# Kernel tuning notes

Measured on AMD Instinct MI355X. Metric: run time of the kernel, lower is better.

## Reference

```python
import jax, jax.numpy as jnp
import numpy as np

N = 50000      # nodes
E = 800000     # edges (before self loops)
D_IN = 128
D_H = 128
HEADS = 4
C = D_H // HEADS
D_OUT = 64
G = 50         # graphs in batch
EPS = 1e-5


def setup_inputs() -> dict:
    key = jax.random.key(0)
    ks = jax.random.split(key, 40)
    def rn(k, shape, scale=0.05):
        return jax.random.normal(k, shape, jnp.float32) * scale
    inp = {}
    inp['x'] = jax.random.normal(ks[0], (N, D_IN), jnp.float32)
    inp['edge_index'] = jax.random.randint(ks[1], (2, E), 0, N, dtype=jnp.int32)
    inp['batch'] = jnp.sort(jax.random.randint(ks[2], (N,), 0, G, dtype=jnp.int32))
    # GATConv 1 (in=D_IN, heads=4, out-per-head=C, concat)
    inp['gat1_W'] = rn(ks[3], (D_IN, D_H))
    inp['gat1_as'] = rn(ks[4], (HEADS, C))
    inp['gat1_ad'] = rn(ks[5], (HEADS, C))
    inp['gat1_b'] = rn(ks[6], (D_H,))
    # GATConv 2 (in=D_H)
    inp['gat2_W'] = rn(ks[7], (D_H, D_H))
    inp['gat2_as'] = rn(ks[8], (HEADS, C))
    inp['gat2_ad'] = rn(ks[9], (HEADS, C))
    inp['gat2_b'] = rn(ks[10], (D_H,))
    # SAGEConv 3/4/5: lin_l (aggregated neighbors, has bias), lin_r (root, no bias)
    for i, kk in zip((3, 4, 5), (11, 14, 17)):
        inp[f'sage{i}_Wl'] = rn(ks[kk], (D_H, D_H))
        inp[f'sage{i}_bl'] = rn(ks[kk + 1], (D_H,))
        inp[f'sage{i}_Wr'] = rn(ks[kk + 2], (D_H, D_H))
    # BatchNorms (training-mode batch statistics)
    for i in range(1, 6):
        inp[f'bn{i}_g'] = jnp.ones((D_H,), jnp.float32)
        inp[f'bn{i}_b'] = jnp.zeros((D_H,), jnp.float32)
    # residual projections + final fc
    inp['res1_W'] = rn(ks[20], (D_IN, D_H)); inp['res1_b'] = rn(ks[21], (D_H,))
    inp['res2_W'] = rn(ks[22], (D_H, D_H)); inp['res2_b'] = rn(ks[23], (D_H,))
    inp['fc_W'] = rn(ks[24], (D_H, D_OUT)); inp['fc_b'] = rn(ks[25], (D_OUT,))
    return inp


def _segsum(v, idx, n):
    return jax.ops.segment_sum(v, idx, num_segments=n)


def _gat(x, W, a_src, a_dst, b, src, dst):
    # PyG GATConv with self loops already appended to (src, dst).
    h = (x @ W).reshape(N, HEADS, C)
    es = jnp.einsum('nhc,hc->nh', h, a_src)           # [N,H]
    ed = jnp.einsum('nhc,hc->nh', h, a_dst)
    e = jax.nn.leaky_relu(es[src] + ed[dst], 0.2)     # [Etot,H]
    m = jax.ops.segment_max(e, dst, num_segments=N)
    m = jnp.where(jnp.isfinite(m), m, 0.0)
    w = jnp.exp(e - m[dst])
    z = _segsum(w, dst, N)
    alpha = w / jnp.maximum(z[dst], 1e-16)            # edge softmax over dst
    out = _segsum(h[src] * alpha[:, :, None], dst, N)  # [N,H,C]
    return out.reshape(N, D_H) + b


def _sage(x, Wl, bl, Wr, src, dst):
    # PyG SAGEConv(aggr='mean'): lin_l(mean_neighbors) + lin_r(x)
    deg = _segsum(jnp.ones((src.shape[0],), x.dtype), dst, N)
    mean = _segsum(x[src], dst, N) / jnp.maximum(deg, 1.0)[:, None]
    return mean @ Wl + bl + x @ Wr


def _bn(x, g, b):
    mu = x.mean(0)
    var = x.var(0)
    return g * (x - mu) * jax.lax.rsqrt(var + EPS) + b


def reference(x, edge_index, batch,
              gat1_W, gat1_as, gat1_ad, gat1_b,
              gat2_W, gat2_as, gat2_ad, gat2_b,
              sage3_Wl, sage3_bl, sage3_Wr,
              sage4_Wl, sage4_bl, sage4_Wr,
              sage5_Wl, sage5_bl, sage5_Wr,
              bn1_g, bn1_b, bn2_g, bn2_b, bn3_g, bn3_b, bn4_g, bn4_b, bn5_g, bn5_b,
              res1_W, res1_b, res2_W, res2_b, fc_W, fc_b):
    src, dst = edge_index[0], edge_index[1]
    loops = jnp.arange(N, dtype=edge_index.dtype)
    gsrc = jnp.concatenate([src, loops])   # GATConv adds self loops by default
    gdst = jnp.concatenate([dst, loops])
    lrelu = lambda v: jax.nn.leaky_relu(v, 0.2)

    res1 = x @ res1_W + res1_b
    h = _gat(x, gat1_W, gat1_as, gat1_ad, gat1_b, gsrc, gdst)
    h = lrelu(_bn(h, bn1_g, bn1_b) + res1)            # dropout = identity (eval)

    res2 = h @ res2_W + res2_b
    h = _gat(h, gat2_W, gat2_as, gat2_ad, gat2_b, gsrc, gdst)
    h = lrelu(_bn(h, bn2_g, bn2_b) + res2)

    h = lrelu(_bn(_sage(h, sage3_Wl, sage3_bl, sage3_Wr, src, dst), bn3_g, bn3_b))
    h = lrelu(_bn(_sage(h, sage4_Wl, sage4_bl, sage4_Wr, src, dst), bn4_g, bn4_b))
    h = lrelu(_bn(_sage(h, sage5_Wl, sage5_bl, sage5_Wr, src, dst), bn5_g, bn5_b))

    # global_mean_pool over graphs
    cnt = jax.ops.segment_sum(jnp.ones((N,), h.dtype), batch, num_segments=G)
    pooled = jax.ops.segment_sum(h, batch, num_segments=G) / jnp.maximum(cnt, 1.0)[:, None]
    return pooled @ fc_W + fc_b
```

## Files before the change

### kernel.cpp

```cpp
#include <hip/hip_runtime.h>
#include <math.h>
#include <stdint.h>

#define N_NODES 50000
#define N_EDGES 800000
#define D 128
#define GR 50
#define EPSV 1e-5f

typedef __attribute__((ext_vector_type(8))) short bf16x8;
typedef __attribute__((ext_vector_type(4))) float f32x4;

__device__ __forceinline__ float lrelu(float v){ return v > 0.f ? v : 0.2f*v; }

__device__ __forceinline__ unsigned int f2bf(float f){
  union { float f; uint32_t i; } v; v.f = f;
  uint32_t r = v.i + 0x7fffu + ((v.i >> 16) & 1u);
  return r >> 16;
}
__device__ __forceinline__ float2 bf2f2(uint32_t u){
  union { uint32_t i; float f; } a, b;
  a.i = u << 16;
  b.i = u & 0xffff0000u;
  return make_float2(a.f, b.f);
}

__global__ void k_countrank(const int* __restrict__ dst, int* __restrict__ deg,
                            int* __restrict__ rank){
  int e = blockIdx.x*256 + threadIdx.x;
  if (e < N_EDGES) rank[e] = atomicAdd(&deg[dst[e]], 1);
}
__global__ void k_scan1(const int* __restrict__ deg, int* __restrict__ bsum){
  __shared__ int s[256];
  int i = blockIdx.x*256 + threadIdx.x;
  int v = (i < N_NODES) ? deg[i] : 0;
  s[threadIdx.x] = v; __syncthreads();
  for (int off = 128; off > 0; off >>= 1){
    if (threadIdx.x < off) s[threadIdx.x] += s[threadIdx.x + off];
    __syncthreads();
  }
  if (threadIdx.x == 0) bsum[blockIdx.x] = s[0];
}
__global__ void k_scan2b(int* __restrict__ bsum, int nb, int* __restrict__ rowStart){
  __shared__ int s[256];
  int t = threadIdx.x;
  int v = (t < nb) ? bsum[t] : 0;
  s[t] = v; __syncthreads();
  for (int off = 1; off < 256; off <<= 1){
    int xv = (t >= off) ? s[t - off] : 0;
    __syncthreads();
    s[t] += xv;
    __syncthreads();
  }
  if (t < nb) bsum[t] = s[t] - v;
  if (t == 255) rowStart[N_NODES] = s[255];
}
__global__ void k_scan3(const int* __restrict__ deg, const int* __restrict__ bsum,
                        int* __restrict__ rowStart){
  __shared__ int s[256];
  int i = blockIdx.x*256 + threadIdx.x;
  int v = (i < N_NODES) ? deg[i] : 0;
  s[threadIdx.x] = v; __syncthreads();
  for (int off = 1; off < 256; off <<= 1){
    int xv = (threadIdx.x >= off) ? s[threadIdx.x - off] : 0;
    __syncthreads();
    s[threadIdx.x] += xv;
    __syncthreads();
  }
  if (i < N_NODES) rowStart[i] = bsum[blockIdx.x] + s[threadIdx.x] - v;
}
__global__ void k_scatter(const int* __restrict__ src, const int* __restrict__ dst,
                          const int* __restrict__ rank, const int* __restrict__ rowStart,
                          int* __restrict__ srcList){
  int e = blockIdx.x*256 + threadIdx.x;
  if (e < N_EDGES)
    srcList[rowStart[dst[e]] + rank[e]] = src[e];
}

__global__ void k_cast_x(const float* __restrict__ x, unsigned short* __restrict__ x16){
  int idx = blockIdx.x*256 + threadIdx.x;
  if (idx >= N_NODES*32) return;
  float4 v = *(const float4*)(x + (size_t)idx*4);
  uint2 pk;
  pk.x = f2bf(v.x) | (f2bf(v.y) << 16);
  pk.y = f2bf(v.z) | (f2bf(v.w) << 16);
  *(uint2*)(x16 + (size_t)idx*4) = pk;
}

struct WPack { const float* w[10]; };
__global__ void k_castw(WPack p, unsigned short* __restrict__ wt){
  int mat = blockIdx.x >> 6;
  int local = (blockIdx.x & 63)*256 + threadIdx.x;
  int c = local >> 7, k = local & 127;
  wt[(size_t)mat*16384 + c*128 + k] = (unsigned short)f2bf(p.w[mat][k*128 + c]);
}

__device__ __forceinline__ void stage_w(const unsigned short* __restrict__ wt,
                                        unsigned short* __restrict__ lds, int t){
  #pragma unroll
  for (int i = 0; i < 8; ++i){
    int ch = i*256 + t;
    int col = ch >> 4, kc = ch & 15;
    *(uint4*)(&lds[col*136 + kc*8]) = *(const uint4*)(wt + ((size_t)col << 7) + (kc << 3));
  }
}

__device__ __forceinline__ void mfma_k128(const unsigned short* __restrict__ xrow,
                                          const unsigned short* __restrict__ lds,
                                          int lane, f32x4 acc[8]){
  int quad = lane >> 4, m = lane & 15;
  #pragma unroll
  for (int ks = 0; ks < 4; ++ks){
    bf16x8 a = *(const bf16x8*)(xrow + ks*32 + quad*8);
    #pragma unroll
    for (int nt = 0; nt < 8; ++nt){
      bf16x8 b = *(const bf16x8*)(&lds[(nt*16 + m)*136 + ks*32 + quad*8]);
      acc[nt] = __builtin_amdgcn_mfma_f32_16x16x32_bf16(a, b, acc[nt], 0, 0, 0);
    }
  }
}

__global__ __launch_bounds__(256) void k_mgemm(const unsigned short* __restrict__ X16,
    const unsigned short* __restrict__ wt, const float* __restrict__ bias,
    float* __restrict__ Y, int n){
  __shared__ __align__(16) unsigned short Wlds[128*136];
  int t = threadIdx.x, lane = t & 63, w = t >> 6;
  int quad = lane >> 4, m = lane & 15;
  int rbase = blockIdx.x*64 + w*16;
  stage_w(wt, Wlds, t);
  f32x4 acc[8];
  #pragma unroll
  for (int nt = 0; nt < 8; ++nt){ acc[nt][0]=0.f; acc[nt][1]=0.f; acc[nt][2]=0.f; acc[nt][3]=0.f; }
  int rowA = rbase + m; if (rowA >= n) rowA = n - 1;
  __syncthreads();
  mfma_k128(X16 + (size_t)rowA*128, Wlds, lane, acc);
  #pragma unroll
  for (int nt = 0; nt < 8; ++nt){
    int col = nt*16 + m;
    float bv = bias[col];
    #pragma unroll
    for (int reg = 0; reg < 4; ++reg){
      int row = rbase + quad*4 + reg;
      if (row < n) Y[(size_t)row*128 + col] = acc[nt][reg] + bv;
    }
  }
}

__global__ __launch_bounds__(256) void k_mgemm_gat(const unsigned short* __restrict__ X16,
    const unsigned short* __restrict__ wt, const float* __restrict__ as_,
    const float* __restrict__ ad_, unsigned short* __restrict__ H16,
    float* __restrict__ es, float* __restrict__ ed, int n){
  __shared__ __align__(16) unsigned short Wlds[128*136];
  int t = threadIdx.x, lane = t & 63, w = t >> 6;
  int quad = lane >> 4, m = lane & 15;
  int rbase = blockIdx.x*64 + w*16;
  stage_w(wt, Wlds, t);
  f32x4 acc[8];
  #pragma unroll
  for (int nt = 0; nt < 8; ++nt){ acc[nt][0]=0.f; acc[nt][1]=0.f; acc[nt][2]=0.f; acc[nt][3]=0.f; }
  int rowA = rbase + m; if (rowA >= n) rowA = n - 1;
  __syncthreads();
  mfma_k128(X16 + (size_t)rowA*128, Wlds, lane, acc);

  float asv[8], adv[8];
  #pragma unroll
  for (int nt = 0; nt < 8; ++nt){ asv[nt] = as_[nt*16 + m]; adv[nt] = ad_[nt*16 + m]; }

  #pragma unroll
  for (int reg = 0; reg < 4; ++reg){
    int row = rbase + quad*4 + reg;
    float pe[4], pd[4];
    #pragma unroll
    for (int h = 0; h < 4; ++h){
      pe[h] = acc[2*h][reg]*asv[2*h] + acc[2*h+1][reg]*asv[2*h+1];
      pd[h] = acc[2*h][reg]*adv[2*h] + acc[2*h+1][reg]*adv[2*h+1];
    }
    #pragma unroll
    for (int h = 0; h < 4; ++h){
      pe[h] += __shfl_xor(pe[h], 1); pe[h] += __shfl_xor(pe[h], 2);
      pe[h] += __shfl_xor(pe[h], 4); pe[h] += __shfl_xor(pe[h], 8);
      pd[h] += __shfl_xor(pd[h], 1); pd[h] += __shfl_xor(pd[h], 2);
      pd[h] += __shfl_xor(pd[h], 4); pd[h] += __shfl_xor(pd[h], 8);
    }
    if (m == 0 && row < n){
      #pragma unroll
      for (int h = 0; h < 4; ++h){ es[row*4 + h] = pe[h]; ed[row*4 + h] = pd[h]; }
    }
  }
  #pragma unroll
  for (int nt = 0; nt < 8; ++nt){
    int col = nt*16 + m;
    #pragma unroll
    for (int reg = 0; reg < 4; ++reg){
      int row = rbase + quad*4 + reg;
      if (row < n) H16[(size_t)row*128 + col] = (unsigned short)f2bf(acc[nt][reg]);
    }
  }
}

__global__ __launch_bounds__(256) void k_mgemm2(const unsigned short* __restrict__ Xa,
    const unsigned short* __restrict__ wta, const unsigned short* __restrict__ Xb,
    const unsigned short* __restrict__ wtb, const float* __restrict__ bias,
    float* __restrict__ Y, int n, float* __restrict__ bnsum){
  __shared__ __align__(16) unsigned short Wlds[128*136];
  __shared__ float redS[128], redQ[128];
  int t = threadIdx.x, lane = t & 63, w = t >> 6;
  int quad = lane >> 4, m = lane & 15;
  int rbase = blockIdx.x*64 + w*16;
  if (t < 128){ redS[t] = 0.f; redQ[t] = 0.f; }
  f32x4 acc[8];
  #pragma unroll
  for (int nt = 0; nt < 8; ++nt){ acc[nt][0]=0.f; acc[nt][1]=0.f; acc[nt][2]=0.f; acc[nt][3]=0.f; }
  int rowA = rbase + m; if (rowA >= n) rowA = n - 1;

  stage_w(wta, Wlds, t);
  __syncthreads();
  mfma_k128(Xa + (size_t)rowA*128, Wlds, lane, acc);
  __syncthreads();
  stage_w(wtb, Wlds, t);
  __syncthreads();
  mfma_k128(Xb + (size_t)rowA*128, Wlds, lane, acc);

  #pragma unroll
  for (int nt = 0; nt < 8; ++nt){
    int col = nt*16 + m;
    float bv = bias[col];
    float s = 0.f, q = 0.f;
    #pragma unroll
    for (int reg = 0; reg < 4; ++reg){
      int row = rbase + quad*4 + reg;
      if (row < n){
        float o = acc[nt][reg] + bv;
        Y[(size_t)row*128 + col] = o;
        s += o; q += o*o;
      }
    }
    atomicAdd(&redS[col], s);
    atomicAdd(&redQ[col], q);
  }
  __syncthreads();
  if (t < 128){
    atomicAdd(&bnsum[t],       redS[t]);
    atomicAdd(&bnsum[128 + t], redQ[t]);
  }
}

__global__ __launch_bounds__(256) void k_gat(const unsigned int* __restrict__ h16,
    const float* __restrict__ es, const float* __restrict__ edv,
    const int* __restrict__ rowStart, const int* __restrict__ srcList,
    const float* __restrict__ bias, float* __restrict__ out){
  int i = blockIdx.x*4 + (threadIdx.x >> 6);
  if (i >= N_NODES) return;
  int lane = threadIdx.x & 63;
  int hd = lane >> 4;
  int c  = lane * 2;
  float edi = edv[i*4 + hd];
  float2 self = bf2f2(h16[(size_t)i*64 + lane]);
  float w = __expf(lrelu(es[i*4 + hd] + edi));
  float z = w, acc0 = self.x*w, acc1 = self.y*w;
  int k0 = rowStart[i], ke = rowStart[i + 1];
  int k = k0;
  for (; k + 7 < ke; k += 8){
    int s[8]; uint32_t u[8]; float ev[8];
    #pragma unroll
    for (int j = 0; j < 8; ++j) s[j] = srcList[k + j];
    #pragma unroll
    for (int j = 0; j < 8; ++j) u[j] = h16[(size_t)s[j]*64 + lane];
    #pragma unroll
    for (int j = 0; j < 8; ++j) ev[j] = es[s[j]*4 + hd];
    #pragma unroll
    for (int j = 0; j < 8; ++j){
      float wj = __expf(lrelu(ev[j] + edi));
      float2 v = bf2f2(u[j]);
      z += wj; acc0 += v.x*wj; acc1 += v.y*wj;
    }
  }
  for (; k < ke; ++k){
    int s0 = srcList[k];
    uint32_t u0 = h16[(size_t)s0*64 + lane];
    float w0 = __expf(lrelu(es[s0*4 + hd] + edi));
    float2 v0 = bf2f2(u0);
    z += w0; acc0 += v0.x*w0; acc1 += v0.y*w0;
  }
  float inv = 1.f / z;
  float2 bv = *(const float2*)(bias + c);
  *(float2*)(out + (size_t)i*D + c) = make_float2(acc0*inv + bv.x, acc1*inv + bv.y);
}

__global__ __launch_bounds__(256) void k_sage_mean(const unsigned int* __restrict__ h16,
    const int* __restrict__ rowStart, const int* __restrict__ srcList,
    unsigned int* __restrict__ out16){
  int i = blockIdx.x*4 + (threadIdx.x >> 6);
  if (i >= N_NODES) return;
  int lane = threadIdx.x & 63;
  int k0 = rowStart[i], k1 = rowStart[i + 1];
  float a0 = 0.f, a1 = 0.f;
  int k = k0;
  for (; k + 7 < k1; k += 8){
    int s[8]; uint32_t u[8];
    #pragma unroll
    for (int j = 0; j < 8; ++j) s[j] = srcList[k + j];
    #pragma unroll
    for (int j = 0; j < 8; ++j) u[j] = h16[(size_t)s[j]*64 + lane];
    #pragma unroll
    for (int j = 0; j < 8; ++j){
      float2 v = bf2f2(u[j]);
      a0 += v.x; a1 += v.y;
    }
  }
  for (; k < k1; ++k){
    uint32_t u0 = h16[(size_t)srcList[k]*64 + lane];
    float2 v0 = bf2f2(u0);
    a0 += v0.x; a1 += v0.y;
  }
  int dg = k1 - k0;
  float inv = 1.f / (float)(dg > 0 ? dg : 1);
  out16[(size_t)i*64 + lane] = f2bf(a0*inv) | (f2bf(a1*inv) << 16);
}

__global__ __launch_bounds__(256) void k_bnstat(const float* __restrict__ x,
                                                float* __restrict__ sums){
  int col = threadIdx.x & 127;
  int ro  = threadIdx.x >> 7;
  float s = 0.f, s2 = 0.f;
  for (int r = blockIdx.x*2 + ro; r < N_NODES; r += gridDim.x*2){
    float v = x[(size_t)r*D + col];
    s += v; s2 += v*v;
  }
  __shared__ float rs[256], rq[256];
  rs[threadIdx.x] = s; rq[threadIdx.x] = s2;
  __syncthreads();
  if (threadIdx.x < 128){
    atomicAdd(&sums[col],       rs[threadIdx.x] + rs[threadIdx.x + 128]);
    atomicAdd(&sums[128 + col], rq[threadIdx.x] + rq[threadIdx.x + 128]);
  }
}

__global__ void k_bnapply(const float* __restrict__ x, const float* __restrict__ sums,
    const float* __restrict__ g, const float* __restrict__ b,
    const float* __restrict__ res, float* __restrict__ y,
    unsigned int* __restrict__ y16){
  int f = blockIdx.x*256 + threadIdx.x;
  if (f >= N_NODES*32) return;
  int c = (f & 31) * 4;
  float4 v = *(const float4*)(x + (size_t)f*4);
  float vv[4] = {v.x, v.y, v.z, v.w};
  float rr[4] = {0.f, 0.f, 0.f, 0.f};
  if (res){
    float4 rv = *(const float4*)(res + (size_t)f*4);
    rr[0]=rv.x; rr[1]=rv.y; rr[2]=rv.z; rr[3]=rv.w;
  }
  float o[4];
  const float invn = 1.f / (float)N_NODES;
  #pragma unroll
  for (int j = 0; j < 4; ++j){
    int cc = c + j;
    float mu  = sums[cc] * invn;
    float var = sums[128 + cc] * invn - mu*mu;
    float rs  = rsqrtf(var + EPSV);
    o[j] = lrelu((vv[j] - mu)*rs*g[cc] + b[cc] + rr[j]);
  }
  if (y) *(float4*)(y + (size_t)f*4) = make_float4(o[0], o[1], o[2], o[3]);
  if (y16){
    uint2 pk;
    pk.x = f2bf(o[0]) | (f2bf(o[1]) << 16);
    pk.y = f2bf(o[2]) | (f2bf(o[3]) << 16);
    *(uint2*)(y16 + (size_t)f*2) = pk;
  }
}

__global__ __launch_bounds__(256) void k_pool(const float* __restrict__ h,
    const int* __restrict__ batch, float* __restrict__ pooled,
    float* __restrict__ cnt){
  int col = threadIdx.x & 127;
  int ro  = threadIdx.x >> 7;
  int base = blockIdx.x * 128;
  int g_cur = -1; float acc = 0.f, cacc = 0.f;
  for (int ii = 0; ii < 64; ++ii){
    int r = base + ro + ii*2;
    if (r >= N_NODES) break;
    int g = batch[r];
    if (g != g_cur){
      if (g_cur >= 0){
        atomicAdd(&pooled[g_cur*D + col], acc);
        if (col == 0) atomicAdd(&cnt[g_cur], cacc);
      }
      acc = 0.f; cacc = 0.f; g_cur = g;
    }
    acc  += h[(size_t)r*D + col];
    cacc += 1.f;
  }
  if (g_cur >= 0){
    atomicAdd(&pooled[g_cur*D + col], acc);
    if (col == 0) atomicAdd(&cnt[g_cur], cacc);
  }
}

__global__ void k_fc(const float* __restrict__ pooled, const float* __restrict__ cnt,
    const float* __restrict__ W, const float* __restrict__ b, float* __restrict__ out){
  int idx = blockIdx.x*256 + threadIdx.x;
  if (idx >= GR*64) return;
  int g = idx >> 6, o = idx & 63;
  const float* p = pooled + g*D;
  float s = 0.f;
  for (int c2 = 0; c2 < D; ++c2) s += p[c2] * W[c2*64 + o];
  float inv = 1.f / fmaxf(cnt[g], 1.f);
  out[idx] = s*inv + b[o];
}

extern "C" void kernel_launch(void* const* d_in, const int* in_sizes, int n_in,
                              void* d_out, int out_size, void* d_ws, size_t ws_size,
                              hipStream_t stream){
  (void)in_sizes; (void)n_in; (void)out_size; (void)ws_size;
  const float* x       = (const float*)d_in[0];
  const int*   ei      = (const int*)  d_in[1];
  const int*   batch   = (const int*)  d_in[2];
  const float* gat1_W  = (const float*)d_in[3];
  const float* gat1_as = (const float*)d_in[4];
  const float* gat1_ad = (const float*)d_in[5];
  const float* gat1_b  = (const float*)d_in[6];
  const float* gat2_W  = (const float*)d_in[7];
  const float* gat2_as = (const float*)d_in[8];
  const float* gat2_ad = (const float*)d_in[9];
  const float* gat2_b  = (const float*)d_in[10];
  const float* s3_Wl   = (const float*)d_in[11];
  const float* s3_bl   = (const float*)d_in[12];
  const float* s3_Wr   = (const float*)d_in[13];
  const float* s4_Wl   = (const float*)d_in[14];
  const float* s4_bl   = (const float*)d_in[15];
  const float* s4_Wr   = (const float*)d_in[16];
  const float* s5_Wl   = (const float*)d_in[17];
  const float* s5_bl   = (const float*)d_in[18];
  const float* s5_Wr   = (const float*)d_in[19];
  const float* bn1_g = (const float*)d_in[20]; const float* bn1_b = (const float*)d_in[21];
  const float* bn2_g = (const float*)d_in[22]; const float* bn2_b = (const float*)d_in[23];
  const float* bn3_g = (const float*)d_in[24]; const float* bn3_b = (const float*)d_in[25];
  const float* bn4_g = (const float*)d_in[26]; const float* bn4_b = (const float*)d_in[27];
  const float* bn5_g = (const float*)d_in[28]; const float* bn5_b = (const float*)d_in[29];
  const float* res1_W = (const float*)d_in[30]; const float* res1_b = (const float*)d_in[31];
  const float* res2_W = (const float*)d_in[32]; const float* res2_b = (const float*)d_in[33];
  const float* fc_W   = (const float*)d_in[34]; const float* fc_b   = (const float*)d_in[35];
  float* out = (float*)d_out;

  char* ws = (char*)d_ws;
  size_t off = 0;
  auto alloc = [&](size_t bytes) -> void* {
    void* p = ws + off; off += (bytes + 255) & ~(size_t)255; return p;
  };
  int*   rowStart = (int*)  alloc((N_NODES + 1) * 4);
  int*   deg      = (int*)  alloc((size_t)N_NODES * 4);
  int*   rank     = (int*)  alloc((size_t)N_EDGES * 4);
  int*   srcList  = (int*)  alloc((size_t)N_EDGES * 4);
  int*   bsum     = (int*)  alloc(256 * 4);
  float* bnsums   = (float*)alloc(5 * 256 * 4);
  float* pooled   = (float*)alloc(GR * D * 4);
  float* cnt      = (float*)alloc(64 * 4);
  float* es       = (float*)alloc((size_t)N_NODES * 4 * 4);
  float* edv      = (float*)alloc((size_t)N_NODES * 4 * 4);
  unsigned short* Wt16 = (unsigned short*)alloc(10 * 16384 * 2);
  unsigned short* HX   = (unsigned short*)alloc((size_t)N_NODES * D * 2);
  unsigned short* H16a = (unsigned short*)alloc((size_t)N_NODES * D * 2);
  float* B1 = (float*)alloc((size_t)N_NODES * D * 4);
  float* B3 = (float*)alloc((size_t)N_NODES * D * 4);

  const int* srcE = ei;
  const int* dstE = ei + N_EDGES;
  const int nb = (N_NODES + 255) / 256;
  const int egrid = (N_EDGES + 255) / 256;
  const int mgrid = (N_NODES + 63) / 64;
  const int agrid = (N_NODES + 3) / 4;
  const int bgrid = (N_NODES*32 + 255) / 256;
  const int pgrid = (N_NODES + 127) / 128;

  hipMemsetAsync(deg, 0, (size_t)N_NODES*4, stream);
  hipMemsetAsync(bnsums, 0, (5*256 + GR*D + 64)*4, stream);
  k_countrank<<<egrid, 256, 0, stream>>>(dstE, deg, rank);
  k_scan1<<<nb, 256, 0, stream>>>(deg, bsum);
  k_scan2b<<<1, 256, 0, stream>>>(bsum, nb, rowStart);
  k_scan3<<<nb, 256, 0, stream>>>(deg, bsum, rowStart);
  k_scatter<<<egrid, 256, 0, stream>>>(srcE, dstE, rank, rowStart, srcList);

  WPack wp;
  wp.w[0]=res1_W; wp.w[1]=gat1_W; wp.w[2]=res2_W; wp.w[3]=gat2_W;
  wp.w[4]=s3_Wl;  wp.w[5]=s3_Wr;  wp.w[6]=s4_Wl;  wp.w[7]=s4_Wr;
  wp.w[8]=s5_Wl;  wp.w[9]=s5_Wr;
  k_castw<<<640, 256, 0, stream>>>(wp, Wt16);
  k_cast_x<<<bgrid, 256, 0, stream>>>(x, HX);

  k_mgemm<<<mgrid, 256, 0, stream>>>(HX, Wt16 + 0*16384, res1_b, B1, N_NODES);
  k_mgemm_gat<<<mgrid, 256, 0, stream>>>(HX, Wt16 + 1*16384, gat1_as, gat1_ad,
                                         H16a, es, edv, N_NODES);
  k_gat<<<agrid, 256, 0, stream>>>((const unsigned int*)H16a, es, edv, rowStart, srcList, gat1_b, B3);
  k_bnstat<<<256, 256, 0, stream>>>(B3, bnsums);
  k_bnapply<<<bgrid, 256, 0, stream>>>(B3, bnsums, bn1_g, bn1_b, B1,
                                       nullptr, (unsigned int*)H16a);

  k_mgemm<<<mgrid, 256, 0, stream>>>(H16a, Wt16 + 2*16384, res2_b, B1, N_NODES);
  k_mgemm_gat<<<mgrid, 256, 0, stream>>>(H16a, Wt16 + 3*16384, gat2_as, gat2_ad,
                                         HX, es, edv, N_NODES);
  k_gat<<<agrid, 256, 0, stream>>>((const unsigned int*)HX, es, edv, rowStart, srcList, gat2_b, B3);
  k_bnstat<<<256, 256, 0, stream>>>(B3, bnsums + 256);
  k_bnapply<<<bgrid, 256, 0, stream>>>(B3, bnsums + 256, bn2_g, bn2_b, B1,
                                       nullptr, (unsigned int*)H16a);

  k_sage_mean<<<agrid, 256, 0, stream>>>((const unsigned int*)H16a, rowStart, srcList,
                                         (unsigned int*)HX);
  k_mgemm2<<<mgrid, 256, 0, stream>>>(HX, Wt16 + 4*16384, H16a, Wt16 + 5*16384,
                                      s3_bl, B1, N_NODES, bnsums + 512);
  k_bnapply<<<bgrid, 256, 0, stream>>>(B1, bnsums + 512, bn3_g, bn3_b, nullptr,
                                       nullptr, (unsigned int*)H16a);

  k_sage_mean<<<agrid, 256, 0, stream>>>((const unsigned int*)H16a, rowStart, srcList,
                                         (unsigned int*)HX);
  k_mgemm2<<<mgrid, 256, 0, stream>>>(HX, Wt16 + 6*16384, H16a, Wt16 + 7*16384,
                                      s4_bl, B1, N_NODES, bnsums + 768);
  k_bnapply<<<bgrid, 256, 0, stream>>>(B1, bnsums + 768, bn4_g, bn4_b, nullptr,
                                       nullptr, (unsigned int*)H16a);

  k_sage_mean<<<agrid, 256, 0, stream>>>((const unsigned int*)H16a, rowStart, srcList,
                                         (unsigned int*)HX);
  k_mgemm2<<<mgrid, 256, 0, stream>>>(HX, Wt16 + 8*16384, H16a, Wt16 + 9*16384,
                                      s5_bl, B1, N_NODES, bnsums + 1024);
  k_bnapply<<<bgrid, 256, 0, stream>>>(B1, bnsums + 1024, bn5_g, bn5_b, nullptr,
                                       B3, nullptr);

  k_pool<<<pgrid, 256, 0, stream>>>(B3, batch, pooled, cnt);
  k_fc<<<(GR*64 + 255)/256, 256, 0, stream>>>(pooled, cnt, fc_W, fc_b, out);
}
```

Before: 728.0 us.

## Store intermediate activations in bf16 and coalesce GEMM epilogues through LDS

```diff
diff --git a/kernel.cpp b/kernel.cpp
--- a/kernel.cpp
+++ b/kernel.cpp
@@ -95,6 +95,7 @@
   wt[(size_t)mat*16384 + c*128 + k] = (unsigned short)f2bf(p.w[mat][k*128 + c]);
 }
 
+
 __device__ __forceinline__ void stage_w(const unsigned short* __restrict__ wt,
                                         unsigned short* __restrict__ lds, int t){
   #pragma unroll
@@ -105,45 +106,67 @@
   }
 }
 
-__device__ __forceinline__ void mfma_k128(const unsigned short* __restrict__ xrow,
+__device__ __forceinline__ void load_a(const unsigned short* __restrict__ xrow,
+                                       int quad, bf16x8 a[4]){
+  #pragma unroll
+  for (int ks = 0; ks < 4; ++ks)
+    a[ks] = *(const bf16x8*)(xrow + ks*32 + quad*8);
+}
+
+__device__ __forceinline__ void mfma_regs(const bf16x8 a[4],
                                           const unsigned short* __restrict__ lds,
                                           int lane, f32x4 acc[8]){
   int quad = lane >> 4, m = lane & 15;
   #pragma unroll
   for (int ks = 0; ks < 4; ++ks){
-    bf16x8 a = *(const bf16x8*)(xrow + ks*32 + quad*8);
     #pragma unroll
     for (int nt = 0; nt < 8; ++nt){
       bf16x8 b = *(const bf16x8*)(&lds[(nt*16 + m)*136 + ks*32 + quad*8]);
-      acc[nt] = __builtin_amdgcn_mfma_f32_16x16x32_bf16(a, b, acc[nt], 0, 0, 0);
-    }
+      acc[nt] = __builtin_amdgcn_mfma_f32_16x16x32_bf16(a[ks], b, acc[nt], 0, 0, 0);
+    }
+  }
+}
+
+__device__ __forceinline__ void epi_store16(f32x4 acc[8], const float* bias,
+    unsigned short* __restrict__ ldsw, unsigned short* __restrict__ Y16,
+    int rbase, int lane, int n){
+  int quad = lane >> 4, m = lane & 15;
+  #pragma unroll
+  for (int nt = 0; nt < 8; ++nt){
+    int col = nt*16 + m;
+    float bv = bias ? bias[col] : 0.f;
+    #pragma unroll
+    for (int reg = 0; reg < 4; ++reg)
+      ldsw[(quad*4 + reg)*132 + col] = (unsigned short)f2bf(acc[nt][reg] + bv);
+  }
+  int r = lane >> 2, seg = lane & 3;
+  int grow = rbase + r;
+  if (grow < n){
+    unsigned short* gp = Y16 + (size_t)grow*128 + seg*32;
+    #pragma unroll
+    for (int j = 0; j < 4; ++j)
+      *(uint4*)(gp + j*8) = *(const uint4*)(&ldsw[r*132 + seg*32 + j*8]);
   }
 }
 
 __global__ __launch_bounds__(256) void k_mgemm(const unsigned short* __restrict__ X16,
     const unsigned short* __restrict__ wt, const float* __restrict__ bias,
-    float* __restrict__ Y, int n){
+    unsigned short* __restrict__ Y16, int n){
   __shared__ __align__(16) unsigned short Wlds[128*136];
   int t = threadIdx.x, lane = t & 63, w = t >> 6;
   int quad = lane >> 4, m = lane & 15;
   int rbase = blockIdx.x*64 + w*16;
+  int rowA = rbase + m; if (rowA >= n) rowA = n - 1;
+  bf16x8 a[4];
+  load_a(X16 + (size_t)rowA*128, quad, a);
   stage_w(wt, Wlds, t);
   f32x4 acc[8];
   #pragma unroll
   for (int nt = 0; nt < 8; ++nt){ acc[nt][0]=0.f; acc[nt][1]=0.f; acc[nt][2]=0.f; acc[nt][3]=0.f; }
-  int rowA = rbase + m; if (rowA >= n) rowA = n - 1;
-  __syncthreads();
-  mfma_k128(X16 + (size_t)rowA*128, Wlds, lane, acc);
-  #pragma unroll
-  for (int nt = 0; nt < 8; ++nt){
-    int col = nt*16 + m;
-    float bv = bias[col];
-    #pragma unroll
-    for (int reg = 0; reg < 4; ++reg){
-      int row = rbase + quad*4 + reg;
-      if (row < n) Y[(size_t)row*128 + col] = acc[nt][reg] + bv;
-    }
-  }
+  __syncthreads();
+  mfma_regs(a, Wlds, lane, acc);
+  __syncthreads();
+  epi_store16(acc, bias, Wlds + w*2112, Y16, rbase, lane, n);
 }
 
 __global__ __launch_bounds__(256) void k_mgemm_gat(const unsigned short* __restrict__ X16,
@@ -154,18 +177,19 @@
   int t = threadIdx.x, lane = t & 63, w = t >> 6;
   int quad = lane >> 4, m = lane & 15;
   int rbase = blockIdx.x*64 + w*16;
+  int rowA = rbase + m; if (rowA >= n) rowA = n - 1;
+  bf16x8 a[4];
+  load_a(X16 + (size_t)rowA*128, quad, a);
   stage_w(wt, Wlds, t);
   f32x4 acc[8];
   #pragma unroll
   for (int nt = 0; nt < 8; ++nt){ acc[nt][0]=0.f; acc[nt][1]=0.f; acc[nt][2]=0.f; acc[nt][3]=0.f; }
-  int rowA = rbase + m; if (rowA >= n) rowA = n - 1;
-  __syncthreads();
-  mfma_k128(X16 + (size_t)rowA*128, Wlds, lane, acc);
+  __syncthreads();
+  mfma_regs(a, Wlds, lane, acc);
 
   float asv[8], adv[8];
   #pragma unroll
   for (int nt = 0; nt < 8; ++nt){ asv[nt] = as_[nt*16 + m]; adv[nt] = ad_[nt*16 + m]; }
-
   #pragma unroll
   for (int reg = 0; reg < 4; ++reg){
     int row = rbase + quad*4 + reg;
@@ -187,68 +211,80 @@
       for (int h = 0; h < 4; ++h){ es[row*4 + h] = pe[h]; ed[row*4 + h] = pd[h]; }
     }
   }
-  #pragma unroll
-  for (int nt = 0; nt < 8; ++nt){
-    int col = nt*16 + m;
-    #pragma unroll
-    for (int reg = 0; reg < 4; ++reg){
-      int row = rbase + quad*4 + reg;
-      if (row < n) H16[(size_t)row*128 + col] = (unsigned short)f2bf(acc[nt][reg]);
-    }
-  }
+  __syncthreads();
+  epi_store16(acc, nullptr, Wlds + w*2112, H16, rbase, lane, n);
 }
 
 __global__ __launch_bounds__(256) void k_mgemm2(const unsigned short* __restrict__ Xa,
     const unsigned short* __restrict__ wta, const unsigned short* __restrict__ Xb,
     const unsigned short* __restrict__ wtb, const float* __restrict__ bias,
-    float* __restrict__ Y, int n, float* __restrict__ bnsum){
+    unsigned short* __restrict__ Y16, int n, float* __restrict__ bnpart){
   __shared__ __align__(16) unsigned short Wlds[128*136];
-  __shared__ float redS[128], redQ[128];
+  __shared__ float wredS[4][128], wredQ[4][128];
   int t = threadIdx.x, lane = t & 63, w = t >> 6;
   int quad = lane >> 4, m = lane & 15;
   int rbase = blockIdx.x*64 + w*16;
-  if (t < 128){ redS[t] = 0.f; redQ[t] = 0.f; }
+  int rowA = rbase + m; if (rowA >= n) rowA = n - 1;
+  bf16x8 aa[4], ab[4];
+  load_a(Xa + (size_t)rowA*128, quad, aa);
+  load_a(Xb + (size_t)rowA*128, quad, ab);
+  stage_w(wta, Wlds, t);
   f32x4 acc[8];
   #pragma unroll
   for (int nt = 0; nt < 8; ++nt){ acc[nt][0]=0.f; acc[nt][1]=0.f; acc[nt][2]=0.f; acc[nt][3]=0.f; }
-  int rowA = rbase + m; if (rowA >= n) rowA = n - 1;
-
-  stage_w(wta, Wlds, t);
-  __syncthreads();
-  mfma_k128(Xa + (size_t)rowA*128, Wlds, lane, acc);
+  __syncthreads();
+  mfma_regs(aa, Wlds, lane, acc);
   __syncthreads();
   stage_w(wtb, Wlds, t);
   __syncthreads();
-  mfma_k128(Xb + (size_t)rowA*128, Wlds, lane, acc);
-
+  mfma_regs(ab, Wlds, lane, acc);
+
+  float colS[8], colQ[8];
   #pragma unroll
   for (int nt = 0; nt < 8; ++nt){
-    int col = nt*16 + m;
-    float bv = bias[col];
+    float bv = bias[nt*16 + m];
     float s = 0.f, q = 0.f;
     #pragma unroll
     for (int reg = 0; reg < 4; ++reg){
-      int row = rbase + quad*4 + reg;
-      if (row < n){
-        float o = acc[nt][reg] + bv;
-        Y[(size_t)row*128 + col] = o;
-        s += o; q += o*o;
-      }
-    }
-    atomicAdd(&redS[col], s);
-    atomicAdd(&redQ[col], q);
+      float o = acc[nt][reg] + bv;
+      acc[nt][reg] = o;
+      if (rbase + quad*4 + reg < n){ s += o; q += o*o; }
+    }
+    s += __shfl_xor(s, 16); s += __shfl_xor(s, 32);
+    q += __shfl_xor(q, 16); q += __shfl_xor(q, 32);
+    colS[nt] = s; colQ[nt] = q;
+  }
+  if (quad == 0){
+    #pragma unroll
+    for (int nt = 0; nt < 8; ++nt){
+      wredS[w][nt*16 + m] = colS[nt];
+      wredQ[w][nt*16 + m] = colQ[nt];
+    }
   }
   __syncthreads();
   if (t < 128){
-    atomicAdd(&bnsum[t],       redS[t]);
-    atomicAdd(&bnsum[128 + t], redQ[t]);
-  }
+    float S = wredS[0][t] + wredS[1][t] + wredS[2][t] + wredS[3][t];
+    float Q = wredQ[0][t] + wredQ[1][t] + wredQ[2][t] + wredQ[3][t];
+    bnpart[(size_t)blockIdx.x*256 + t]       = S;
+    bnpart[(size_t)blockIdx.x*256 + 128 + t] = Q;
+  }
+  epi_store16(acc, nullptr, Wlds + w*2112, Y16, rbase, lane, n);
+}
+
+__global__ void k_bnred(const float* __restrict__ part, int nblk,
+                        float* __restrict__ sums){
+  int g = blockIdx.x, t = threadIdx.x;
+  int chunk = (nblk + 63) / 64;
+  int b0 = g*chunk, b1 = min(nblk, b0 + chunk);
+  float s = 0.f;
+  for (int b = b0; b < b1; ++b) s += part[(size_t)b*256 + t];
+  if (b0 < b1) atomicAdd(&sums[t], s);
 }
 
 __global__ __launch_bounds__(256) void k_gat(const unsigned int* __restrict__ h16,
     const float* __restrict__ es, const float* __restrict__ edv,
     const int* __restrict__ rowStart, const int* __restrict__ srcList,
-    const float* __restrict__ bias, float* __restrict__ out){
+    const float* __restrict__ bias, unsigned int* __restrict__ out16){
   int i = blockIdx.x*4 + (threadIdx.x >> 6);
   if (i >= N_NODES) return;
   int lane = threadIdx.x & 63;
@@ -284,7 +320,7 @@
   }
   float inv = 1.f / z;
   float2 bv = *(const float2*)(bias + c);
-  *(float2*)(out + (size_t)i*D + c) = make_float2(acc0*inv + bv.x, acc1*inv + bv.y);
+  out16[(size_t)i*64 + lane] = f2bf(acc0*inv + bv.x) | (f2bf(acc1*inv + bv.y) << 16);
 }
 
 __global__ __launch_bounds__(256) void k_sage_mean(const unsigned int* __restrict__ h16,
@@ -309,8 +345,7 @@
     }
   }
   for (; k < k1; ++k){
-    uint32_t u0 = h16[(size_t)srcList[k]*64 + lane];
-    float2 v0 = bf2f2(u0);
+    float2 v0 = bf2f2(h16[(size_t)srcList[k]*64 + lane]);
     a0 += v0.x; a1 += v0.y;
   }
   int dg = k1 - k0;
@@ -318,37 +353,46 @@
   out16[(size_t)i*64 + lane] = f2bf(a0*inv) | (f2bf(a1*inv) << 16);
 }
 
-__global__ __launch_bounds__(256) void k_bnstat(const float* __restrict__ x,
+__global__ __launch_bounds__(256) void k_bnstat(const unsigned int* __restrict__ x16,
                                                 float* __restrict__ sums){
-  int col = threadIdx.x & 127;
-  int ro  = threadIdx.x >> 7;
-  float s = 0.f, s2 = 0.f;
-  for (int r = blockIdx.x*2 + ro; r < N_NODES; r += gridDim.x*2){
-    float v = x[(size_t)r*D + col];
-    s += v; s2 += v*v;
-  }
-  __shared__ float rs[256], rq[256];
-  rs[threadIdx.x] = s; rq[threadIdx.x] = s2;
-  __syncthreads();
-  if (threadIdx.x < 128){
-    atomicAdd(&sums[col],       rs[threadIdx.x] + rs[threadIdx.x + 128]);
-    atomicAdd(&sums[128 + col], rq[threadIdx.x] + rq[threadIdx.x + 128]);
-  }
-}
-
-__global__ void k_bnapply(const float* __restrict__ x, const float* __restrict__ sums,
-    const float* __restrict__ g, const float* __restrict__ b,
-    const float* __restrict__ res, float* __restrict__ y,
+  int colu = threadIdx.x & 63;
+  int ro   = threadIdx.x >> 6;
+  float s0 = 0.f, s1 = 0.f, q0 = 0.f, q1 = 0.f;
+  for (int r = blockIdx.x*4 + ro; r < N_NODES; r += gridDim.x*4){
+    float2 v = bf2f2(x16[(size_t)r*64 + colu]);
+    s0 += v.x; s1 += v.y; q0 += v.x*v.x; q1 += v.y*v.y;
+  }
+  __shared__ float rs0[256], rs1[256], rq0[256], rq1[256];
+  int t = threadIdx.x;
+  rs0[t] = s0; rs1[t] = s1; rq0[t] = q0; rq1[t] = q1;
+  __syncthreads();
+  if (t < 64){
+    float S0 = rs0[t] + rs0[t+64] + rs0[t+128] + rs0[t+192];
+    float S1 = rs1[t] + rs1[t+64] + rs1[t+128] + rs1[t+192];
+    float Q0 = rq0[t] + rq0[t+64] + rq0[t+128] + rq0[t+192];
+    float Q1 = rq1[t] + rq1[t+64] + rq1[t+128] + rq1[t+192];
+    atomicAdd(&sums[2*t],       S0);
+    atomicAdd(&sums[2*t + 1],   S1);
+    atomicAdd(&sums[128 + 2*t],     Q0);
+    atomicAdd(&sums[128 + 2*t + 1], Q1);
+  }
+}
+
+__global__ void k_bnapply(const unsigned int* __restrict__ x16,
+    const float* __restrict__ sums, const float* __restrict__ g,
+    const float* __restrict__ b, const unsigned int* __restrict__ res16,
     unsigned int* __restrict__ y16){
   int f = blockIdx.x*256 + threadIdx.x;
   if (f >= N_NODES*32) return;
   int c = (f & 31) * 4;
-  float4 v = *(const float4*)(x + (size_t)f*4);
-  float vv[4] = {v.x, v.y, v.z, v.w};
+  uint2 u = *(const uint2*)(x16 + (size_t)f*2);
+  float2 vA = bf2f2(u.x), vB = bf2f2(u.y);
+  float vv[4] = {vA.x, vA.y, vB.x, vB.y};
   float rr[4] = {0.f, 0.f, 0.f, 0.f};
-  if (res){
-    float4 rv = *(const float4*)(res + (size_t)f*4);
-    rr[0]=rv.x; rr[1]=rv.y; rr[2]=rv.z; rr[3]=rv.w;
+  if (res16){
+    uint2 ur = *(const uint2*)(res16 + (size_t)f*2);
+    float2 rA = bf2f2(ur.x), rB = bf2f2(ur.y);
+    rr[0]=rA.x; rr[1]=rA.y; rr[2]=rB.x; rr[3]=rB.y;
   }
   float o[4];
   const float invn = 1.f / (float)N_NODES;
@@ -360,39 +404,38 @@
     float rs  = rsqrtf(var + EPSV);
     o[j] = lrelu((vv[j] - mu)*rs*g[cc] + b[cc] + rr[j]);
   }
-  if (y) *(float4*)(y + (size_t)f*4) = make_float4(o[0], o[1], o[2], o[3]);
-  if (y16){
-    uint2 pk;
-    pk.x = f2bf(o[0]) | (f2bf(o[1]) << 16);
-    pk.y = f2bf(o[2]) | (f2bf(o[3]) << 16);
-    *(uint2*)(y16 + (size_t)f*2) = pk;
-  }
-}
-
-__global__ __launch_bounds__(256) void k_pool(const float* __restrict__ h,
+  uint2 pk;
+  pk.x = f2bf(o[0]) | (f2bf(o[1]) << 16);
+  pk.y = f2bf(o[2]) | (f2bf(o[3]) << 16);
+  *(uint2*)(y16 + (size_t)f*2) = pk;
+}
+
+__global__ __launch_bounds__(256) void k_pool(const unsigned int* __restrict__ h16,
     const int* __restrict__ batch, float* __restrict__ pooled,
     float* __restrict__ cnt){
-  int col = threadIdx.x & 127;
-  int ro  = threadIdx.x >> 7;
+  int colu = threadIdx.x & 63;
+  int ro   = threadIdx.x >> 6;
   int base = blockIdx.x * 128;
-  int g_cur = -1; float acc = 0.f, cacc = 0.f;
-  for (int ii = 0; ii < 64; ++ii){
-    int r = base + ro + ii*2;
+  int g_cur = -1; float a0 = 0.f, a1 = 0.f, cacc = 0.f;
+  for (int ii = 0; ii < 32; ++ii){
+    int r = base + ro + ii*4;
     if (r >= N_NODES) break;
     int g = batch[r];
     if (g != g_cur){
       if (g_cur >= 0){
-        atomicAdd(&pooled[g_cur*D + col], acc);
-        if (col == 0) atomicAdd(&cnt[g_cur], cacc);
+        atomicAdd(&pooled[g_cur*D + 2*colu],     a0);
+        atomicAdd(&pooled[g_cur*D + 2*colu + 1], a1);
+        if (colu == 0) atomicAdd(&cnt[g_cur], cacc);
       }
-      acc = 0.f; cacc = 0.f; g_cur = g;
-    }
-    acc  += h[(size_t)r*D + col];
-    cacc += 1.f;
+      a0 = 0.f; a1 = 0.f; cacc = 0.f; g_cur = g;
+    }
+    float2 v = bf2f2(h16[(size_t)r*64 + colu]);
+    a0 += v.x; a1 += v.y; cacc += 1.f;
   }
   if (g_cur >= 0){
-    atomicAdd(&pooled[g_cur*D + col], acc);
-    if (col == 0) atomicAdd(&cnt[g_cur], cacc);
+    atomicAdd(&pooled[g_cur*D + 2*colu],     a0);
+    atomicAdd(&pooled[g_cur*D + 2*colu + 1], a1);
+    if (colu == 0) atomicAdd(&cnt[g_cur], cacc);
   }
 }
 
@@ -447,6 +490,7 @@
   auto alloc = [&](size_t bytes) -> void* {
     void* p = ws + off; off += (bytes + 255) & ~(size_t)255; return p;
   };
+  const int mgrid = (N_NODES + 63) / 64;
   int*   rowStart = (int*)  alloc((N_NODES + 1) * 4);
   int*   deg      = (int*)  alloc((size_t)N_NODES * 4);
   int*   rank     = (int*)  alloc((size_t)N_EDGES * 4);
@@ -457,17 +501,17 @@
   float* cnt      = (float*)alloc(64 * 4);
   float* es       = (float*)alloc((size_t)N_NODES * 4 * 4);
   float* edv      = (float*)alloc((size_t)N_NODES * 4 * 4);
+  float* bnpart   = (float*)alloc((size_t)mgrid * 256 * 4);
   unsigned short* Wt16 = (unsigned short*)alloc(10 * 16384 * 2);
   unsigned short* HX   = (unsigned short*)alloc((size_t)N_NODES * D * 2);
   unsigned short* H16a = (unsigned short*)alloc((size_t)N_NODES * D * 2);
-  float* B1 = (float*)alloc((size_t)N_NODES * D * 4);
-  float* B3 = (float*)alloc((size_t)N_NODES * D * 4);
+  unsigned short* HO   = (unsigned short*)alloc((size_t)N_NODES * D * 2);
+  unsigned short* HR   = (unsigned short*)alloc((size_t)N_NODES * D * 2);
 
   const int* srcE = ei;
   const int* dstE = ei + N_EDGES;
   const int nb = (N_NODES + 255) / 256;
   const int egrid = (N_EDGES + 255) / 256;
-  const int mgrid = (N_NODES + 63) / 64;
   const int agrid = (N_NODES + 3) / 4;
   const int bgrid = (N_NODES*32 + 255) / 256;
   const int pgrid = (N_NODES + 127) / 128;
@@ -487,43 +531,48 @@
   k_castw<<<640, 256, 0, stream>>>(wp, Wt16);
   k_cast_x<<<bgrid, 256, 0, stream>>>(x, HX);
 
-  k_mgemm<<<mgrid, 256, 0, stream>>>(HX, Wt16 + 0*16384, res1_b, B1, N_NODES);
+  k_mgemm<<<mgrid, 256, 0, stream>>>(HX, Wt16 + 0*16384, res1_b, HR, N_NODES);
   k_mgemm_gat<<<mgrid, 256, 0, stream>>>(HX, Wt16 + 1*16384, gat1_as, gat1_ad,
                                          H16a, es, edv, N_NODES);
-  k_gat<<<agrid, 256, 0, stream>>>((const unsigned int*)H16a, es, edv, rowStart, srcList, gat1_b, B3);
-  k_bnstat<<<256, 256, 0, stream>>>(B3, bnsums);
-  k_bnapply<<<bgrid, 256, 0, stream>>>(B3, bnsums, bn1_g, bn1_b, B1,
-                                       nullptr, (unsigned int*)H16a);
-
-  k_mgemm<<<mgrid, 256, 0, stream>>>(H16a, Wt16 + 2*16384, res2_b, B1, N_NODES);
+  k_gat<<<agrid, 256, 0, stream>>>((const unsigned int*)H16a, es, edv, rowStart,
+                                   srcList, gat1_b, (unsigned int*)HO);
+  k_bnstat<<<256, 256, 0, stream>>>((const unsigned int*)HO, bnsums);
+  k_bnapply<<<bgrid, 256, 0, stream>>>((const unsigned int*)HO, bnsums, bn1_g, bn1_b,
+                                       (const unsigned int*)HR, (unsigned int*)H16a);
+
+  k_mgemm<<<mgrid, 256, 0, stream>>>(H16a, Wt16 + 2*16384, res2_b, HR, N_NODES);
   k_mgemm_gat<<<mgrid, 256, 0, stream>>>(H16a, Wt16 + 3*16384, gat2_as, gat2_ad,
                                          HX, es, edv, N_NODES);
-  k_gat<<<agrid, 256, 0, stream>>>((const unsigned int*)HX, es, edv, rowStart, srcList, gat2_b, B3);
-  k_bnstat<<<256, 256, 0, stream>>>(B3, bnsums + 256);
-  k_bnapply<<<bgrid, 256, 0, stream>>>(B3, bnsums + 256, bn2_g, bn2_b, B1,
-                                       nullptr, (unsigned int*)H16a);
+  k_gat<<<agrid, 256, 0, stream>>>((const unsigned int*)HX, es, edv, rowStart,
+                                   srcList, gat2_b, (unsigned int*)HO);
+  k_bnstat<<<256, 256, 0, stream>>>((const unsigned int*)HO, bnsums + 256);
+  k_bnapply<<<bgrid, 256, 0, stream>>>((const unsigned int*)HO, bnsums + 256, bn2_g, bn2_b,
+                                       (const unsigned int*)HR, (unsigned int*)H16a);
 
   k_sage_mean<<<agrid, 256, 0, stream>>>((const unsigned int*)H16a, rowStart, srcList,
                                          (unsigned int*)HX);
   k_mgemm2<<<mgrid, 256, 0, stream>>>(HX, Wt16 + 4*16384, H16a, Wt16 + 5*16384,
-                                      s3_bl, B1, N_NODES, bnsums + 512);
-  k_bnapply<<<bgrid, 256, 0, stream>>>(B1, bnsums + 512, bn3_g, bn3_b, nullptr,
+                                      s3_bl, HO, N_NODES, bnpart);
+  k_bnred<<<64, 256, 0, stream>>>(bnpart, mgrid, bnsums + 512);
+  k_bnapply<<<bgrid, 256, 0, stream>>>((const unsigned int*)HO, bnsums + 512, bn3_g, bn3_b,
                                        nullptr, (unsigned int*)H16a);
 
   k_sage_mean<<<agrid, 256, 0, stream>>>((const unsigned int*)H16a, rowStart, srcList,
                                          (unsigned int*)HX);
   k_mgemm2<<<mgrid, 256, 0, stream>>>(HX, Wt16 + 6*16384, H16a, Wt16 + 7*16384,
-                                      s4_bl, B1, N_NODES, bnsums + 768);
-  k_bnapply<<<bgrid, 256, 0, stream>>>(B1, bnsums + 768, bn4_g, bn4_b, nullptr,
+                                      s4_bl, HO, N_NODES, bnpart);
+  k_bnred<<<64, 256, 0, stream>>>(bnpart, mgrid, bnsums + 768);
+  k_bnapply<<<bgrid, 256, 0, stream>>>((const unsigned int*)HO, bnsums + 768, bn4_g, bn4_b,
                                        nullptr, (unsigned int*)H16a);
 
   k_sage_mean<<<agrid, 256, 0, stream>>>((const unsigned int*)H16a, rowStart, srcList,
                                          (unsigned int*)HX);
   k_mgemm2<<<mgrid, 256, 0, stream>>>(HX, Wt16 + 8*16384, H16a, Wt16 + 9*16384,
-                                      s5_bl, B1, N_NODES, bnsums + 1024);
-  k_bnapply<<<bgrid, 256, 0, stream>>>(B1, bnsums + 1024, bn5_g, bn5_b, nullptr,
-                                       B3, nullptr);
-
-  k_pool<<<pgrid, 256, 0, stream>>>(B3, batch, pooled, cnt);
+                                      s5_bl, HO, N_NODES, bnpart);
+  k_bnred<<<64, 256, 0, stream>>>(bnpart, mgrid, bnsums + 1024);
+  k_bnapply<<<bgrid, 256, 0, stream>>>((const unsigned int*)HO, bnsums + 1024, bn5_g, bn5_b,
+                                       nullptr, (unsigned int*)H16a);
+
+  k_pool<<<pgrid, 256, 0, stream>>>((const unsigned int*)H16a, batch, pooled, cnt);
   k_fc<<<(GR*64 + 255)/256, 256, 0, stream>>>(pooled, cnt, fc_W, fc_b, out);
 }
```

Result: faster. 653.5 us (-10.2%).
